# Optimization experiments

Measured on AMD Instinct MI355X. Metric: run time of the kernel, lower is better.

## Reference

```python
import jax, jax.numpy as jnp
import numpy as np

EMBED = 256
NHEAD = 8
HDIM = EMBED // NHEAD
EPS = 1e-6


def setup_inputs() -> dict:
    key = jax.random.key(0)
    ks = jax.random.split(key, 10)
    B, L, E = 8, 8192, EMBED
    sc = 1.0 / np.sqrt(E)
    return {
        "q": jax.random.normal(ks[0], (B, L, E), jnp.float32),
        "k": jax.random.normal(ks[1], (B, L, E), jnp.float32),
        "v": jax.random.normal(ks[2], (B, L, E), jnp.float32),
        "Wq": jax.random.normal(ks[3], (E, E), jnp.float32) * sc,
        "bq": jax.random.normal(ks[4], (E,), jnp.float32) * 0.01,
        "Wk": jax.random.normal(ks[5], (E, E), jnp.float32) * sc,
        "bk": jax.random.normal(ks[6], (E,), jnp.float32) * 0.01,
        "Wv": jax.random.normal(ks[7], (E, E), jnp.float32) * sc,
        "bv": jax.random.normal(ks[8], (E,), jnp.float32) * 0.01,
        "Wm": jax.random.normal(ks[9], (E, E), jnp.float32) * sc,
    }


def _feature_map(x):
    # elu(x) + 1, the LoFTR linear-attention kernel feature map
    return jax.nn.elu(x) + 1.0


def reference(q, k, v, Wq, bq, Wk, bk, Wv, bv, Wm):
    B, L, E = q.shape
    # QKV projections (nn.Linear: x @ W.T + b), split into heads
    Q = (q @ Wq.T + bq).reshape(B, L, NHEAD, HDIM)
    K = (k @ Wk.T + bk).reshape(B, -1, NHEAD, HDIM)
    V = (v @ Wv.T + bv).reshape(B, -1, NHEAD, HDIM)

    Qf = _feature_map(Q)              # [B,L,H,D]
    Kf = _feature_map(K)              # [B,S,H,D]
    v_len = V.shape[1]
    Vn = V / v_len
    # KV: per-head outer-product accumulation over source positions
    KV = jnp.einsum("bshd,bshv->bhdv", Kf, Vn)       # [B,H,D,D]
    Ksum = Kf.sum(axis=1)                              # [B,H,D]
    Z = 1.0 / (jnp.einsum("blhd,bhd->blh", Qf, Ksum) + EPS)  # [B,L,H]
    msg = jnp.einsum("blhd,bhdv,blh->blhv", Qf, KV, Z) * v_len  # [B,L,H,D]
    # merge heads and output projection (bias=False)
    out = msg.reshape(B, L, NHEAD * HDIM) @ Wm.T
    return out
```

## Files before the change

### kernel.cpp

```cpp
#include <hip/hip_runtime.h>
#include <hip/hip_bf16.h>

#define SEQ   8192
#define NB    8
#define EMB   256
#define NHD   8
#define HDM   32

typedef __attribute__((ext_vector_type(8))) short short8;
typedef __attribute__((ext_vector_type(4))) float floatx4;
typedef __attribute__((ext_vector_type(16))) float floatx16;

__device__ __forceinline__ short f2b(float f) {
    __hip_bfloat16 h = __float2bfloat16(f);
    return __builtin_bit_cast(short, h);
}
__device__ __forceinline__ float b2f(short s) {
    unsigned u = (unsigned)(unsigned short)s << 16;
    return __builtin_bit_cast(float, u);
}

template <int MODE>
__launch_bounds__(256)
__global__ void proj_kernel(const float* __restrict__ X,
                            const float* __restrict__ W,
                            const float* __restrict__ bias,
                            short* __restrict__ out,
                            float* __restrict__ Ksum) {
    __shared__ __align__(16) short As[128 * 64];
    __shared__ __align__(16) short Bs[128 * 64];
    __shared__ float colsum[128];

    const int tid  = threadIdx.x;
    const int tm   = blockIdx.x;
    const int tn   = blockIdx.y;
    const int lane = tid & 63;
    const int wave = tid >> 6;
    const int wm   = (wave & 1) << 6;
    const int wn   = (wave >> 1) << 6;
    const int fr   = lane & 15;
    const int fq   = lane >> 4;

    if (MODE == 1 && tid < 128) colsum[tid] = 0.f;

    floatx4 acc[4][4];
    #pragma unroll
    for (int i = 0; i < 4; i++)
        #pragma unroll
        for (int j = 0; j < 4; j++)
            #pragma unroll
            for (int r = 0; r < 4; r++) acc[i][j][r] = 0.f;

    const int r  = tid >> 1;
    const int c0 = (tid & 1) << 5;
    const float* ap = X + (size_t)(tm * 128 + r) * EMB + c0;
    const float* bp = W + (size_t)(tn * 128 + r) * EMB + c0;

    for (int kc = 0; kc < 4; kc++) {
        const int kb = kc * 64;
        #pragma unroll
        for (int u = 0; u < 8; u++) {
            float4 f = *(const float4*)(ap + kb + 4 * u);
            short4 ha = make_short4(f2b(f.x), f2b(f.y), f2b(f.z), f2b(f.w));
            *(short4*)&As[r * 64 + c0 + 4 * u] = ha;
            float4 g = *(const float4*)(bp + kb + 4 * u);
            short4 hb = make_short4(f2b(g.x), f2b(g.y), f2b(g.z), f2b(g.w));
            *(short4*)&Bs[r * 64 + c0 + 4 * u] = hb;
        }
        __syncthreads();
        #pragma unroll
        for (int kk = 0; kk < 64; kk += 32) {
            short8 a[4], b[4];
            #pragma unroll
            for (int i = 0; i < 4; i++)
                a[i] = *(const short8*)&As[(wm + i * 16 + fr) * 64 + kk + fq * 8];
            #pragma unroll
            for (int j = 0; j < 4; j++)
                b[j] = *(const short8*)&Bs[(wn + j * 16 + fr) * 64 + kk + fq * 8];
            #pragma unroll
            for (int i = 0; i < 4; i++)
                #pragma unroll
                for (int j = 0; j < 4; j++)
                    acc[i][j] = __builtin_amdgcn_mfma_f32_16x16x32_bf16(a[i], b[j], acc[i][j], 0, 0, 0);
        }
        __syncthreads();
    }

    const int row0 = tm * 128;
    float ks[4] = {0.f, 0.f, 0.f, 0.f};
    #pragma unroll
    for (int i = 0; i < 4; i++) {
        #pragma unroll
        for (int j = 0; j < 4; j++) {
            const int colg = tn * 128 + wn + j * 16 + fr;
            const float bia = bias[colg];
            #pragma unroll
            for (int rr = 0; rr < 4; rr++) {
                const int rowg = row0 + wm + i * 16 + fq * 4 + rr;
                float v = acc[i][j][rr] + bia;
                if (MODE <= 1) v = (v > 0.f) ? (v + 1.f) : __expf(v);
                else           v *= (1.0f / (float)SEQ);
                out[(size_t)rowg * EMB + colg] = f2b(v);
                if (MODE == 1) ks[j] += v;
            }
        }
    }
    if (MODE == 1) {
        #pragma unroll
        for (int j = 0; j < 4; j++)
            atomicAdd(&colsum[wn + j * 16 + fr], ks[j]);
        __syncthreads();
        if (tid < 128) {
            const int b = (tm * 128) / SEQ;
            atomicAdd(&Ksum[b * EMB + tn * 128 + tid], colsum[tid]);
        }
    }
}

template <bool ATOMIC>
__launch_bounds__(256)
__global__ void kv_kernel(const short* __restrict__ Kf,
                          const short* __restrict__ Vn,
                          float* __restrict__ dst_base,
                          int kvsp) {
    __shared__ __align__(16) short Kt[32 * 256];
    __shared__ __align__(16) short Vt[32 * 256];

    const int tid  = threadIdx.x;
    const int sp   = blockIdx.x % kvsp;
    const int b    = blockIdx.x / kvsp;
    const int wave = tid >> 6;
    const int lane = tid & 63;
    const int h    = wave * 2 + (lane >> 5);
    const int l5   = lane & 31;
    const int d0   = (l5 >> 2) * 4;
    const int v0   = (l5 & 3) * 8;
    const int chunk = SEQ / kvsp;
    const size_t rowbase = (size_t)(b * SEQ + sp * chunk) * EMB;

    float acc[4][8];
    #pragma unroll
    for (int i = 0; i < 4; i++)
        #pragma unroll
        for (int j = 0; j < 8; j++) acc[i][j] = 0.f;

    for (int t0 = 0; t0 < chunk; t0 += 32) {
        __syncthreads();
        const short* ksrc = Kf + rowbase + (size_t)t0 * EMB;
        const short* vsrc = Vn + rowbase + (size_t)t0 * EMB;
        #pragma unroll
        for (int u = 0; u < 4; u++) {
            const int c   = tid + u * 256;
            const int row = c >> 5;
            const int col = (c & 31) * 8;
            *(short8*)&Kt[row * 256 + col] = *(const short8*)(ksrc + (size_t)row * EMB + col);
            *(short8*)&Vt[row * 256 + col] = *(const short8*)(vsrc + (size_t)row * EMB + col);
        }
        __syncthreads();
        #pragma unroll 4
        for (int s = 0; s < 32; s++) {
            short4 k4 = *(const short4*)&Kt[s * 256 + h * 32 + d0];
            short8 v8 = *(const short8*)&Vt[s * 256 + h * 32 + v0];
            float kf[4] = {b2f(k4.x), b2f(k4.y), b2f(k4.z), b2f(k4.w)};
            float vf[8];
            #pragma unroll
            for (int j = 0; j < 8; j++) vf[j] = b2f(v8[j]);
            #pragma unroll
            for (int i = 0; i < 4; i++)
                #pragma unroll
                for (int j = 0; j < 8; j++) acc[i][j] += kf[i] * vf[j];
        }
    }

    if (ATOMIC) {
        float* dst = dst_base + (size_t)((b * 8 + h) * 1024);
        #pragma unroll
        for (int i = 0; i < 4; i++)
            #pragma unroll
            for (int j = 0; j < 8; j++)
                atomicAdd(&dst[(d0 + i) * 32 + v0 + j], acc[i][j]);
    } else {
        float* dst = dst_base + (size_t)(((size_t)sp * NB + b) * 8 + h) * 1024;
        #pragma unroll
        for (int i = 0; i < 4; i++) {
            float4 lo = make_float4(acc[i][0], acc[i][1], acc[i][2], acc[i][3]);
            float4 hi = make_float4(acc[i][4], acc[i][5], acc[i][6], acc[i][7]);
            *(float4*)&dst[(d0 + i) * 32 + v0]     = lo;
            *(float4*)&dst[(d0 + i) * 32 + v0 + 4] = hi;
        }
    }
}

__launch_bounds__(256)
__global__ void kvred_kernel(const float* __restrict__ KVp,
                             float* __restrict__ KV, int kvsp) {
    const int i = blockIdx.x * 1024 + threadIdx.x * 4;
    float4 s = make_float4(0.f, 0.f, 0.f, 0.f);
    for (int p = 0; p < kvsp; p++) {
        float4 t = *(const float4*)&KVp[(size_t)p * 65536 + i];
        s.x += t.x; s.y += t.y; s.z += t.z; s.w += t.w;
    }
    *(float4*)&KV[i] = s;
}

__launch_bounds__(64)
__global__ void m_kernel(const float* __restrict__ KV,
                         const float* __restrict__ Wm,
                         short* __restrict__ Mt) {
    const int blk  = blockIdx.x;
    const int e0   = (blk & 7) * 32;
    const int h    = (blk >> 3) & 7;
    const int b    = blk >> 6;
    const int lane = threadIdx.x;
    const int l31  = lane & 31;
    const int q    = lane >> 5;

    floatx16 acc;
    #pragma unroll
    for (int i = 0; i < 16; i++) acc[i] = 0.f;

    #pragma unroll
    for (int kb = 0; kb < 32; kb += 16) {
        const float* ar = KV + (size_t)(((b * 8 + h) * 32 + l31) * 32) + kb + q * 8;
        const float* br = Wm + (size_t)(e0 + l31) * EMB + h * 32 + kb + q * 8;
        short8 a, w;
        #pragma unroll
        for (int t = 0; t < 8; t++) { a[t] = f2b(ar[t]); w[t] = f2b(br[t]); }
        acc = __builtin_amdgcn_mfma_f32_32x32x16_bf16(a, w, acc, 0, 0, 0);
    }

    short* mrow = Mt + (size_t)b * EMB * EMB + (size_t)(e0 + l31) * EMB + h * 32;
    #pragma unroll
    for (int r4 = 0; r4 < 4; r4++) {
        const int dbase = 8 * r4 + 4 * q;
        short4 s4 = make_short4(f2b(acc[r4 * 4 + 0]), f2b(acc[r4 * 4 + 1]),
                                f2b(acc[r4 * 4 + 2]), f2b(acc[r4 * 4 + 3]));
        *(short4*)(mrow + dbase) = s4;
    }
}

__launch_bounds__(256)
__global__ void out_kernel(const short* __restrict__ Qf,
                           const float* __restrict__ Ksum,
                           const short* __restrict__ Mt,
                           float* __restrict__ Out) {
    __shared__ __align__(16) short As[128 * 64];
    __shared__ __align__(16) short Bs[128 * 64];
    __shared__ float zs[128][NHD];
    __shared__ float ksl[EMB];

    const int tid  = threadIdx.x;
    const int tm   = blockIdx.x;
    const int tn   = blockIdx.y;
    const int b    = (tm * 128) / SEQ;
    const int lane = tid & 63;
    const int wave = tid >> 6;
    const int wm   = (wave & 1) << 6;
    const int wn   = (wave >> 1) << 6;
    const int fr   = lane & 15;
    const int fq   = lane >> 4;

    ksl[tid] = Ksum[b * EMB + tid];
    __syncthreads();

    {
        const int t  = tid >> 1;
        const int h0 = (tid & 1) * 4;
        const short* qrow = Qf + (size_t)(tm * 128 + t) * EMB;
        #pragma unroll
        for (int hh = 0; hh < 4; hh++) {
            const int h = h0 + hh;
            float d = 0.f;
            #pragma unroll
            for (int u = 0; u < 8; u++) {
                short4 q4 = *(const short4*)(qrow + h * 32 + 4 * u);
                d += b2f(q4.x) * ksl[h * 32 + 4 * u + 0] + b2f(q4.y) * ksl[h * 32 + 4 * u + 1]
                   + b2f(q4.z) * ksl[h * 32 + 4 * u + 2] + b2f(q4.w) * ksl[h * 32 + 4 * u + 3];
            }
            zs[t][h] = (float)SEQ / (d + 1e-6f);
        }
    }
    __syncthreads();

    floatx4 acc[4][4];
    #pragma unroll
    for (int i = 0; i < 4; i++)
        #pragma unroll
        for (int j = 0; j < 4; j++)
            #pragma unroll
            for (int r = 0; r < 4; r++) acc[i][j][r] = 0.f;

    const int r  = tid >> 1;
    const int c0 = (tid & 1) << 5;
    const short* ap = Qf + (size_t)(tm * 128 + r) * EMB + c0;
    const short* bp = Mt + (size_t)b * EMB * EMB + (size_t)(tn * 128 + r) * EMB + c0;

    for (int kc = 0; kc < 4; kc++) {
        const int kb = kc * 64;
        const int h  = (kb + c0) >> 5;
        const float z = zs[r][h];
        #pragma unroll
        for (int u = 0; u < 8; u++) {
            short4 q4 = *(const short4*)(ap + kb + 4 * u);
            short4 oa = make_short4(f2b(b2f(q4.x) * z), f2b(b2f(q4.y) * z),
                                    f2b(b2f(q4.z) * z), f2b(b2f(q4.w) * z));
            *(short4*)&As[r * 64 + c0 + 4 * u] = oa;
            *(short4*)&Bs[r * 64 + c0 + 4 * u] = *(const short4*)(bp + kb + 4 * u);
        }
        __syncthreads();
        #pragma unroll
        for (int kk = 0; kk < 64; kk += 32) {
            short8 a[4], bb[4];
            #pragma unroll
            for (int i = 0; i < 4; i++)
                a[i] = *(const short8*)&As[(wm + i * 16 + fr) * 64 + kk + fq * 8];
            #pragma unroll
            for (int j = 0; j < 4; j++)
                bb[j] = *(const short8*)&Bs[(wn + j * 16 + fr) * 64 + kk + fq * 8];
            #pragma unroll
            for (int i = 0; i < 4; i++)
                #pragma unroll
                for (int j = 0; j < 4; j++)
                    acc[i][j] = __builtin_amdgcn_mfma_f32_16x16x32_bf16(a[i], bb[j], acc[i][j], 0, 0, 0);
        }
        __syncthreads();
    }

    const int row0 = tm * 128;
    #pragma unroll
    for (int i = 0; i < 4; i++) {
        #pragma unroll
        for (int j = 0; j < 4; j++) {
            const int colg = tn * 128 + wn + j * 16 + fr;
            #pragma unroll
            for (int rr = 0; rr < 4; rr++) {
                const int rowg = row0 + wm + i * 16 + fq * 4 + rr;
                Out[(size_t)rowg * EMB + colg] = acc[i][j][rr];
            }
        }
    }
}

extern "C" void kernel_launch(void* const* d_in, const int* in_sizes, int n_in,
                              void* d_out, int out_size, void* d_ws, size_t ws_size,
                              hipStream_t stream) {
    (void)in_sizes; (void)n_in; (void)out_size;
    const float* q  = (const float*)d_in[0];
    const float* k  = (const float*)d_in[1];
    const float* v  = (const float*)d_in[2];
    const float* Wq = (const float*)d_in[3];
    const float* bq = (const float*)d_in[4];
    const float* Wk = (const float*)d_in[5];
    const float* bk = (const float*)d_in[6];
    const float* Wv = (const float*)d_in[7];
    const float* bv = (const float*)d_in[8];
    const float* Wm = (const float*)d_in[9];

    char* ws = (char*)d_ws;
    short* Qf   = (short*)(ws);
    short* Kf   = (short*)(ws + 33554432);
    short* Vn   = (short*)(ws + 67108864);
    float* Ksum = (float*)(ws + 100663296);
    float* KV   = (float*)(ws + 100663296 + 8192);
    short* Mt   = (short*)(ws + 100663296 + 8192 + 262144);
    const size_t kvp_off = 100663296ull + 8192 + 262144 + 1048576;
    float* KVp  = (float*)(ws + kvp_off);

    int kvsp = 0;
    if      (ws_size >= kvp_off + 64ull * 262144) kvsp = 64;
    else if (ws_size >= kvp_off + 32ull * 262144) kvsp = 32;
    else if (ws_size >= kvp_off + 16ull * 262144) kvsp = 16;

    hipMemsetAsync(ws + 100663296, 0, 8192 + 262144, stream);

    dim3 grid(512, 2), blk(256);
    proj_kernel<0><<<grid, blk, 0, stream>>>(q, Wq, bq, Qf, nullptr);
    proj_kernel<1><<<grid, blk, 0, stream>>>(k, Wk, bk, Kf, Ksum);
    proj_kernel<2><<<grid, blk, 0, stream>>>(v, Wv, bv, Vn, nullptr);

    if (kvsp) {
        kv_kernel<false><<<NB * kvsp, 256, 0, stream>>>(Kf, Vn, KVp, kvsp);
        kvred_kernel<<<64, 256, 0, stream>>>(KVp, KV, kvsp);
    } else {
        kv_kernel<true><<<NB * 16, 256, 0, stream>>>(Kf, Vn, KV, 16);
    }

    m_kernel<<<512, 64, 0, stream>>>(KV, Wm, Mt);
    out_kernel<<<grid, blk, 0, stream>>>(Qf, Ksum, Mt, (float*)d_out);
}
```

Before: 429.3 us.

## Merge QKV projections into one launch, pad LDS rows, coalesce tile loads

Folds the three projection launches into one grid with a z dimension that selects q, k or v, so there is a single larger launch. Global-to-LDS loads are remapped so consecutive threads read consecutive 16-byte chunks of a row, giving coalesced access. LDS rows are padded from 64 to 72 elements to cut bank conflicts on the MFMA fragment reads. The mode becomes a runtime value instead of a template argument, which adds some branching and register pressure.

```diff
diff --git a/kernel.cpp b/kernel.cpp
--- a/kernel.cpp
+++ b/kernel.cpp
@@ -6,6 +6,7 @@
 #define EMB   256
 #define NHD   8
 #define HDM   32
+#define LDP   72
 
 typedef __attribute__((ext_vector_type(8))) short short8;
 typedef __attribute__((ext_vector_type(4))) float floatx4;
@@ -20,20 +21,24 @@
     return __builtin_bit_cast(float, u);
 }
 
-template <int MODE>
 __launch_bounds__(256)
-__global__ void proj_kernel(const float* __restrict__ X,
-                            const float* __restrict__ W,
-                            const float* __restrict__ bias,
-                            short* __restrict__ out,
-                            float* __restrict__ Ksum) {
-    __shared__ __align__(16) short As[128 * 64];
-    __shared__ __align__(16) short Bs[128 * 64];
+__global__ void qkv_kernel(const float* __restrict__ qin,
+                           const float* __restrict__ kin,
+                           const float* __restrict__ vin,
+                           const float* __restrict__ Wq, const float* __restrict__ bq,
+                           const float* __restrict__ Wk, const float* __restrict__ bk,
+                           const float* __restrict__ Wv, const float* __restrict__ bv,
+                           short* __restrict__ Qf, short* __restrict__ Kf,
+                           short* __restrict__ Vn,
+                           float* __restrict__ Ksum) {
+    __shared__ __align__(16) short As[128 * LDP];
+    __shared__ __align__(16) short Bs[128 * LDP];
     __shared__ float colsum[128];
 
     const int tid  = threadIdx.x;
     const int tm   = blockIdx.x;
     const int tn   = blockIdx.y;
+    const int mode = blockIdx.z;
     const int lane = tid & 63;
     const int wave = tid >> 6;
     const int wm   = (wave & 1) << 6;
@@ -41,7 +46,12 @@
     const int fr   = lane & 15;
     const int fq   = lane >> 4;
 
-    if (MODE == 1 && tid < 128) colsum[tid] = 0.f;
+    const float* X    = (mode == 0) ? qin : (mode == 1) ? kin : vin;
+    const float* W    = (mode == 0) ? Wq  : (mode == 1) ? Wk  : Wv;
+    const float* bias = (mode == 0) ? bq  : (mode == 1) ? bk  : bv;
+    short*       out  = (mode == 0) ? Qf  : (mode == 1) ? Kf  : Vn;
+
+    if (mode == 1 && tid < 128) colsum[tid] = 0.f;
 
     floatx4 acc[4][4];
     #pragma unroll
@@ -51,21 +61,22 @@
             #pragma unroll
             for (int r = 0; r < 4; r++) acc[i][j][r] = 0.f;
 
-    const int r  = tid >> 1;
-    const int c0 = (tid & 1) << 5;
-    const float* ap = X + (size_t)(tm * 128 + r) * EMB + c0;
-    const float* bp = W + (size_t)(tn * 128 + r) * EMB + c0;
+    const float* Xb = X + (size_t)(tm * 128) * EMB;
+    const float* Wb = W + (size_t)(tn * 128) * EMB;
 
     for (int kc = 0; kc < 4; kc++) {
         const int kb = kc * 64;
         #pragma unroll
         for (int u = 0; u < 8; u++) {
-            float4 f = *(const float4*)(ap + kb + 4 * u);
-            short4 ha = make_short4(f2b(f.x), f2b(f.y), f2b(f.z), f2b(f.w));
-            *(short4*)&As[r * 64 + c0 + 4 * u] = ha;
-            float4 g = *(const float4*)(bp + kb + 4 * u);
-            short4 hb = make_short4(f2b(g.x), f2b(g.y), f2b(g.z), f2b(g.w));
-            *(short4*)&Bs[r * 64 + c0 + 4 * u] = hb;
+            const int g   = u * 256 + tid;
+            const int row = g >> 4;
+            const int c4  = (g & 15) * 4;
+            float4 f = *(const float4*)(Xb + (size_t)row * EMB + kb + c4);
+            *(short4*)&As[row * LDP + c4] =
+                make_short4(f2b(f.x), f2b(f.y), f2b(f.z), f2b(f.w));
+            float4 g4 = *(const float4*)(Wb + (size_t)row * EMB + kb + c4);
+            *(short4*)&Bs[row * LDP + c4] =
+                make_short4(f2b(g4.x), f2b(g4.y), f2b(g4.z), f2b(g4.w));
         }
         __syncthreads();
         #pragma unroll
@@ -73,10 +84,10 @@
             short8 a[4], b[4];
             #pragma unroll
             for (int i = 0; i < 4; i++)
-                a[i] = *(const short8*)&As[(wm + i * 16 + fr) * 64 + kk + fq * 8];
+                a[i] = *(const short8*)&As[(wm + i * 16 + fr) * LDP + kk + fq * 8];
             #pragma unroll
             for (int j = 0; j < 4; j++)
-                b[j] = *(const short8*)&Bs[(wn + j * 16 + fr) * 64 + kk + fq * 8];
+                b[j] = *(const short8*)&Bs[(wn + j * 16 + fr) * LDP + kk + fq * 8];
             #pragma unroll
             for (int i = 0; i < 4; i++)
                 #pragma unroll
@@ -98,14 +109,14 @@
             for (int rr = 0; rr < 4; rr++) {
                 const int rowg = row0 + wm + i * 16 + fq * 4 + rr;
                 float v = acc[i][j][rr] + bia;
-                if (MODE <= 1) v = (v > 0.f) ? (v + 1.f) : __expf(v);
+                if (mode <= 1) v = (v > 0.f) ? (v + 1.f) : __expf(v);
                 else           v *= (1.0f / (float)SEQ);
                 out[(size_t)rowg * EMB + colg] = f2b(v);
-                if (MODE == 1) ks[j] += v;
+                ks[j] += v;
             }
         }
     }
-    if (MODE == 1) {
+    if (mode == 1) {
         #pragma unroll
         for (int j = 0; j < 4; j++)
             atomicAdd(&colsum[wn + j * 16 + fr], ks[j]);
@@ -244,8 +255,8 @@
                            const float* __restrict__ Ksum,
                            const short* __restrict__ Mt,
                            float* __restrict__ Out) {
-    __shared__ __align__(16) short As[128 * 64];
-    __shared__ __align__(16) short Bs[128 * 64];
+    __shared__ __align__(16) short As[128 * LDP];
+    __shared__ __align__(16) short Bs[128 * LDP];
     __shared__ float zs[128][NHD];
     __shared__ float ksl[EMB];
 
@@ -290,22 +301,23 @@
             #pragma unroll
             for (int r = 0; r < 4; r++) acc[i][j][r] = 0.f;
 
-    const int r  = tid >> 1;
-    const int c0 = (tid & 1) << 5;
-    const short* ap = Qf + (size_t)(tm * 128 + r) * EMB + c0;
-    const short* bp = Mt + (size_t)b * EMB * EMB + (size_t)(tn * 128 + r) * EMB + c0;
+    const short* Ab = Qf + (size_t)(tm * 128) * EMB;
+    const short* Bb = Mt + (size_t)b * EMB * EMB + (size_t)(tn * 128) * EMB;
 
     for (int kc = 0; kc < 4; kc++) {
         const int kb = kc * 64;
-        const int h  = (kb + c0) >> 5;
-        const float z = zs[r][h];
-        #pragma unroll
-        for (int u = 0; u < 8; u++) {
-            short4 q4 = *(const short4*)(ap + kb + 4 * u);
-            short4 oa = make_short4(f2b(b2f(q4.x) * z), f2b(b2f(q4.y) * z),
-                                    f2b(b2f(q4.z) * z), f2b(b2f(q4.w) * z));
-            *(short4*)&As[r * 64 + c0 + 4 * u] = oa;
-            *(short4*)&Bs[r * 64 + c0 + 4 * u] = *(const short4*)(bp + kb + 4 * u);
+        #pragma unroll
+        for (int u = 0; u < 4; u++) {
+            const int g   = u * 256 + tid;
+            const int row = g >> 3;
+            const int c8  = (g & 7) * 8;
+            const float z = zs[row][(kb + c8) >> 5];
+            short8 qv = *(const short8*)(Ab + (size_t)row * EMB + kb + c8);
+            short8 oa;
+            #pragma unroll
+            for (int t = 0; t < 8; t++) oa[t] = f2b(b2f(qv[t]) * z);
+            *(short8*)&As[row * LDP + c8] = oa;
+            *(short8*)&Bs[row * LDP + c8] = *(const short8*)(Bb + (size_t)row * EMB + kb + c8);
         }
         __syncthreads();
         #pragma unroll
@@ -313,10 +325,10 @@
             short8 a[4], bb[4];
             #pragma unroll
             for (int i = 0; i < 4; i++)
-                a[i] = *(const short8*)&As[(wm + i * 16 + fr) * 64 + kk + fq * 8];
+                a[i] = *(const short8*)&As[(wm + i * 16 + fr) * LDP + kk + fq * 8];
             #pragma unroll
             for (int j = 0; j < 4; j++)
-                bb[j] = *(const short8*)&Bs[(wn + j * 16 + fr) * 64 + kk + fq * 8];
+                bb[j] = *(const short8*)&Bs[(wn + j * 16 + fr) * LDP + kk + fq * 8];
             #pragma unroll
             for (int i = 0; i < 4; i++)
                 #pragma unroll
@@ -373,10 +385,9 @@
 
     hipMemsetAsync(ws + 100663296, 0, 8192 + 262144, stream);
 
-    dim3 grid(512, 2), blk(256);
-    proj_kernel<0><<<grid, blk, 0, stream>>>(q, Wq, bq, Qf, nullptr);
-    proj_kernel<1><<<grid, blk, 0, stream>>>(k, Wk, bk, Kf, Ksum);
-    proj_kernel<2><<<grid, blk, 0, stream>>>(v, Wv, bv, Vn, nullptr);
+    dim3 blk(256);
+    qkv_kernel<<<dim3(512, 2, 3), blk, 0, stream>>>(q, k, v, Wq, bq, Wk, bk, Wv, bv,
+                                                    Qf, Kf, Vn, Ksum);
 
     if (kvsp) {
         kv_kernel<false><<<NB * kvsp, 256, 0, stream>>>(Kf, Vn, KVp, kvsp);
@@ -386,5 +397,5 @@
     }
 
     m_kernel<<<512, 64, 0, stream>>>(KV, Wm, Mt);
-    out_kernel<<<grid, blk, 0, stream>>>(Qf, Ksum, Mt, (float*)d_out);
-}
+    out_kernel<<<dim3(512, 2), blk, 0, stream>>>(Qf, Ksum, Mt, (float*)d_out);
+}
```

Result: faster. 373.7 us (-13.0%).
